# Kernel optimization log

Measured on AMD Instinct MI355X. Metric: run time of the kernel, lower is better.

The kernel has to match this reference:

```python
import jax, jax.numpy as jnp
import numpy as np

NUM_RELATIONS = 3


def _rgcn(x, W_rel, W_root, bias, src, dst, etype):
    # PyG RGCNConv: out = x @ W_root + bias + sum_r mean_{e: type(e)=r, dst(e)=i} (x_src @ W_r)
    n = x.shape[0]
    xr = jnp.einsum('ni,rio->rno', x, W_rel)          # [R, N, F] relation-transformed nodes
    msg = xr[etype, src]                               # [E, F] per-edge messages
    out = x @ W_root + bias
    for r in range(NUM_RELATIONS):
        m = (etype == r)
        s = jax.ops.segment_sum(jnp.where(m[:, None], msg, 0.0), dst, num_segments=n)
        c = jax.ops.segment_sum(m.astype(x.dtype), dst, num_segments=n)
        out = out + s / jnp.maximum(c, 1.0)[:, None]   # mean aggregation per relation
    return out


def _gate(h, q, Wg, bg, Wq, bq):
    # h: [BN, F], q: [B, L, F]
    B, L, F = q.shape
    N = h.shape[0] // B
    h3 = h.reshape(B, N, F)
    # w_gate(cat([h_i, q_l])) = h_i @ Wg[:, :F].T + q_l @ Wg[:, F:].T + bg
    hg = jnp.einsum('bnf,gf->bng', h3, Wg[:, :F])                    # [B,N,F]
    qg = jnp.einsum('blf,gf->blg', q, Wg[:, F:]) + bg                # [B,L,F]
    attn = jax.nn.sigmoid(hg[:, :, None, :] + qg[:, None, :, :])     # [B,N,L,F]
    qi = jnp.einsum('bnlf,blf->bnf', attn, q)                        # [B,N,F]
    alpha = jax.nn.sigmoid(
        jnp.einsum('bnf,gf->bng', h3, Wq[:, :F])
        + jnp.einsum('bnf,gf->bng', qi, Wq[:, F:]) + bq)
    hn = alpha * jnp.tanh(qi) + (1.0 - alpha) * h3
    return hn.reshape(B * N, F)


def setup_inputs() -> dict:
    key = jax.random.key(0)
    ks = jax.random.split(key, 16)
    F = 768
    BN, E, B, L = 2048, 65536, 8, 64
    s = 0.02
    return {
        'x': jax.random.normal(ks[0], (BN, F), jnp.float32),
        'edge_index': jax.random.randint(ks[1], (2, E), 0, BN),
        'edge_type': jax.random.randint(ks[2], (E,), 0, NUM_RELATIONS),
        'query_embs': jax.random.normal(ks[3], (B, L, F), jnp.float32),
        'W_rel1': jax.random.normal(ks[4], (NUM_RELATIONS, F, F), jnp.float32) * s,
        'W_root1': jax.random.normal(ks[5], (F, F), jnp.float32) * s,
        'b1': jnp.zeros((F,), jnp.float32),
        'W_rel2': jax.random.normal(ks[6], (NUM_RELATIONS, F, F), jnp.float32) * s,
        'W_root2': jax.random.normal(ks[7], (F, F), jnp.float32) * s,
        'b2': jnp.zeros((F,), jnp.float32),
        'Wg': jax.random.normal(ks[8], (F, 2 * F), jnp.float32) * s,
        'bg': jnp.zeros((F,), jnp.float32),
        'Wq': jax.random.normal(ks[9], (F, 2 * F), jnp.float32) * s,
        'bq': jnp.zeros((F,), jnp.float32),
    }


def reference(x, edge_index, edge_type, query_embs,
              W_rel1, W_root1, b1, W_rel2, W_root2, b2, Wg, bg, Wq, bq):
    src, dst = edge_index[0], edge_index[1]
    h = jax.nn.relu(_rgcn(x, W_rel1, W_root1, b1, src, dst, edge_type))
    h = _gate(h, query_embs, Wg, bg, Wq, bq)
    h = jax.nn.relu(_rgcn(h, W_rel2, W_root2, b2, src, dst, edge_type))
    h = _gate(h, query_embs, Wg, bg, Wq, bq)
    return h
```

## Files before the change

### kernel.cpp

```cpp
#include <hip/hip_runtime.h>
#include <hip/hip_bf16.h>
#include <cstdint>
#include <cstddef>

#define F 768

typedef float f32x4 __attribute__((ext_vector_type(4)));
typedef short s16x8 __attribute__((ext_vector_type(8)));
typedef short s16x4 __attribute__((ext_vector_type(4)));

#define NEG_LOG2E (-1.4426950408889634f)

__device__ __forceinline__ float bf2f(unsigned short u) {
  union { unsigned int i; float f; } v; v.i = ((unsigned int)u) << 16; return v.f;
}
__device__ __forceinline__ unsigned short f2bf(float f) {
  union { float f; unsigned int i; } v; v.f = f;
  unsigned int r = v.i + 0x7FFF + ((v.i >> 16) & 1);
  return (unsigned short)(r >> 16);
}

#if __has_builtin(__builtin_amdgcn_exp2f)
__device__ __forceinline__ float fexp2(float x) { return __builtin_amdgcn_exp2f(x); }
#else
__device__ __forceinline__ float fexp2(float x) { return exp2f(x); }
#endif
#if __has_builtin(__builtin_amdgcn_rcpf)
__device__ __forceinline__ float frcp(float x) { return __builtin_amdgcn_rcpf(x); }
#else
__device__ __forceinline__ float frcp(float x) { return 1.0f / x; }
#endif

__device__ __forceinline__ float ftanh(float x) {
  float t = fexp2(x * 2.8853900817779268f);
  float s = frcp(t + 1.0f);
  return fmaf(-2.0f, s, 1.0f);
}
__device__ __forceinline__ float fclamp60(float x) {
  return fminf(fmaxf(x, -60.0f), 60.0f);
}

__device__ __forceinline__ void gload16(const void* g, void* l) {
  __builtin_amdgcn_global_load_lds(
      (const __attribute__((address_space(1))) void*)g,
      (__attribute__((address_space(3))) void*)l, 16, 0, 0);
}

__global__ void khist(const int* __restrict__ ei, int E, int* __restrict__ cnt) {
  int e = blockIdx.x * blockDim.x + threadIdx.x;
  if (e < E) atomicAdd(&cnt[ei[E + e]], 1);
}

__global__ void kscan(const int* __restrict__ cnt, int* __restrict__ offs, int n) {
  __shared__ int part[256];
  int t = threadIdx.x;
  const int per = n / 256;
  int local[8];
  int s = 0;
  for (int j = 0; j < per; ++j) { local[j] = cnt[t * per + j]; s += local[j]; }
  part[t] = s;
  __syncthreads();
  for (int d = 1; d < 256; d <<= 1) {
    int v = (t >= d) ? part[t - d] : 0;
    __syncthreads();
    part[t] += v;
    __syncthreads();
  }
  int run = (t == 0) ? 0 : part[t - 1];
  for (int j = 0; j < per; ++j) { offs[t * per + j] = run; run += local[j]; }
  if (t == 255) offs[n] = run;
}

__global__ void kscatter(const int* __restrict__ ei, const int* __restrict__ et, int E,
                         const int* __restrict__ offs, int* __restrict__ cur,
                         int* __restrict__ sorted) {
  int e = blockIdx.x * blockDim.x + threadIdx.x;
  if (e >= E) return;
  int dst = ei[E + e];
  int pos = offs[dst] + atomicAdd(&cur[dst], 1);
  sorted[pos] = ei[e] | (et[e] << 16);
}

__global__ void kprep(const float* __restrict__ x, const float* __restrict__ q,
                      const float* __restrict__ Wg, const float* __restrict__ Wq,
                      int nx, int nq,
                      unsigned short* __restrict__ Acat, unsigned short* __restrict__ qbf,
                      unsigned short* __restrict__ Wgq, unsigned short* __restrict__ WgR,
                      unsigned short* __restrict__ WqR) {
  const int b = blockIdx.x, c = threadIdx.x * 4;
  const float* srow;
  unsigned short* drow;
  if (b < nx) {
    srow = x + (size_t)b * F; drow = Acat + (size_t)b * 3072;
  } else if (b < nx + nq) {
    srow = q + (size_t)(b - nx) * F; drow = qbf + (size_t)(b - nx) * F;
  } else {
    const int w = b - nx - nq;
    if (w < 1536) {
      srow = (w < 768) ? Wg + (size_t)w * 1536 : Wq + (size_t)(w - 768) * 1536;
      drow = Wgq + (size_t)w * 768;
    } else if (w < 2304) {
      srow = Wg + (size_t)(w - 1536) * 1536 + 768;
      drow = WgR + (size_t)(w - 1536) * 768;
    } else {
      srow = Wq + (size_t)(w - 2304) * 1536 + 768;
      drow = WqR + (size_t)(w - 2304) * 768;
    }
  }
  float4 v = *(const float4*)(srow + c);
  s16x4 o;
  o[0] = (short)f2bf(v.x); o[1] = (short)f2bf(v.y);
  o[2] = (short)f2bf(v.z); o[3] = (short)f2bf(v.w);
  *(s16x4*)(drow + c) = o;
}

__global__ void ktrans(const float* __restrict__ Wr1, const float* __restrict__ Wl1,
                       const float* __restrict__ Wr2, const float* __restrict__ Wl2,
                       unsigned short* __restrict__ Wcat1, unsigned short* __restrict__ Wcat2) {
  __shared__ float tile[64][65];
  const int z = blockIdx.z, layer = z >> 2, part = z & 3;
  const float* src = (part == 0) ? (layer ? Wr2 : Wr1)
                                 : ((layer ? Wl2 : Wl1) + (size_t)(part - 1) * F * F);
  unsigned short* dst = (layer ? Wcat2 : Wcat1) + part * F;
  const int kt = blockIdx.x * 64, nt = blockIdx.y * 64;
  const int t = threadIdx.x, c = t & 63, r4 = t >> 6;
#pragma unroll
  for (int it = 0; it < 16; ++it) {
    int kk = r4 + it * 4;
    tile[kk][c] = src[(size_t)(kt + kk) * F + nt + c];
  }
  __syncthreads();
#pragma unroll
  for (int it = 0; it < 16; ++it) {
    int rr = r4 + it * 4;
    dst[(size_t)(nt + rr) * 3072 + kt + c] = f2bf(tile[c][rr]);
  }
}

__global__ void kagg(const int* __restrict__ offs, const int* __restrict__ sorted,
                     const unsigned short* __restrict__ hin,
                     unsigned short* __restrict__ dst) {
  const int i = blockIdx.x, t = threadIdx.x;
  const int col = t * 4;
  float a0[4] = {}, a1[4] = {}, a2[4] = {};
  int c0 = 0, c1 = 0, c2 = 0;
  const int beg = offs[i], end = offs[i + 1];
  int e = beg;
  for (; e + 3 < end; e += 4) {
    int pk[4];
#pragma unroll
    for (int u = 0; u < 4; ++u) pk[u] = sorted[e + u];
    s16x4 w[4];
#pragma unroll
    for (int u = 0; u < 4; ++u)
      w[u] = *(const s16x4*)(hin + (size_t)(pk[u] & 0xFFFF) * 3072 + col);
#pragma unroll
    for (int u = 0; u < 4; ++u) {
      int r = pk[u] >> 16;
      float v[4];
#pragma unroll
      for (int j = 0; j < 4; ++j) v[j] = bf2f((unsigned short)w[u][j]);
      if (r == 0)      { c0++; for (int j = 0; j < 4; ++j) a0[j] += v[j]; }
      else if (r == 1) { c1++; for (int j = 0; j < 4; ++j) a1[j] += v[j]; }
      else             { c2++; for (int j = 0; j < 4; ++j) a2[j] += v[j]; }
    }
  }
  for (; e < end; ++e) {
    int p0 = sorted[e];
    s16x4 w0 = *(const s16x4*)(hin + (size_t)(p0 & 0xFFFF) * 3072 + col);
    int r0 = p0 >> 16;
    float v0[4];
#pragma unroll
    for (int j = 0; j < 4; ++j) v0[j] = bf2f((unsigned short)w0[j]);
    if (r0 == 0)      { c0++; for (int j = 0; j < 4; ++j) a0[j] += v0[j]; }
    else if (r0 == 1) { c1++; for (int j = 0; j < 4; ++j) a1[j] += v0[j]; }
    else              { c2++; for (int j = 0; j < 4; ++j) a2[j] += v0[j]; }
  }
  const float i0 = frcp((float)(c0 > 0 ? c0 : 1));
  const float i1 = frcp((float)(c1 > 0 ? c1 : 1));
  const float i2 = frcp((float)(c2 > 0 ? c2 : 1));
  unsigned short* d = dst + (size_t)i * 3072 + col;
  s16x4 o;
#pragma unroll
  for (int j = 0; j < 4; ++j) o[j] = (short)f2bf(a0[j] * i0);
  *(s16x4*)d = o;
#pragma unroll
  for (int j = 0; j < 4; ++j) o[j] = (short)f2bf(a1[j] * i1);
  *(s16x4*)(d + F) = o;
#pragma unroll
  for (int j = 0; j < 4; ++j) o[j] = (short)f2bf(a2[j] * i2);
  *(s16x4*)(d + 2 * F) = o;
}

template <int EPI>
__launch_bounds__(512)
__global__ void kmm(const unsigned short* __restrict__ A, int lda,
                    const unsigned short* __restrict__ B, int ldb,
                    float* __restrict__ C, int ldc, int K,
                    const float* __restrict__ bias,
                    const float* __restrict__ auxf,
                    const unsigned short* __restrict__ hbb,
                    unsigned short* __restrict__ C2, int ldc2,
                    unsigned short* __restrict__ tqb,
                    int Lq) {
  __shared__ unsigned short Asb[2][64 * 64];
  __shared__ unsigned short Bsb[2][64 * 64];
  const int t = threadIdx.x;
  const int lane = t & 63, wid = t >> 6;
  const int wr = wid >> 2, wc = wid & 3;
  const int bm = blockIdx.x * 64, bn = blockIdx.y * 64;

  const int srow = t >> 3, schunk = t & 7;
  const int kxor = ((schunk ^ (srow & 7)) << 3);
  const unsigned short* Ap = A + (size_t)(bm + srow) * lda + kxor;
  const unsigned short* Bp = B + (size_t)(bn + srow) * ldb + kxor;

  const int rA0 = wr * 32 + (lane & 15);
  const int rB0 = wc * 16 + (lane & 15);
  const int l7 = lane & 7, lq = lane >> 4;
  const int s8_0 = (((0 * 4 + lq) ^ l7) << 3);
  const int s8_1 = (((1 * 4 + lq) ^ l7) << 3);

  f32x4 acc[2] = {};

  auto stage = [&](int cb, int k0) {
    gload16(Ap + k0, &Asb[cb][t * 8]);
    gload16(Bp + k0, &Bsb[cb][t * 8]);
  };

  stage(0, 0);
  __syncthreads();
  int cur = 0;
  for (int k0 = 0; k0 < K; k0 += 64) {
    if (k0 + 64 < K) stage(cur ^ 1, k0 + 64);
    const unsigned short* As = Asb[cur];
    const unsigned short* Bs = Bsb[cur];
#pragma unroll
    for (int ks = 0; ks < 2; ++ks) {
      const int s8 = ks ? s8_1 : s8_0;
      s16x8 af[2], bf;
#pragma unroll
      for (int i = 0; i < 2; ++i)
        af[i] = *(const s16x8*)(As + (rA0 + i * 16) * 64 + s8);
      bf = *(const s16x8*)(Bs + rB0 * 64 + s8);
#pragma unroll
      for (int i = 0; i < 2; ++i)
        acc[i] = __builtin_amdgcn_mfma_f32_16x16x32_bf16(af[i], bf, acc[i], 0, 0, 0);
    }
    __syncthreads();
    cur ^= 1;
  }

  const int colw = bn + wc * 16 + (lane & 15);

  if (EPI == 7) {
    if (bn < 768) {
      float ea[2][4], qacc[2][4];
#pragma unroll
      for (int i = 0; i < 2; ++i)
#pragma unroll
        for (int j = 0; j < 4; ++j) {
          ea[i][j] = fexp2(fclamp60(acc[i][j] * NEG_LOG2E));
          qacc[i][j] = 0.0f;
        }
      const int b = bm >> 8;
      const float* qb = auxf + (size_t)b * Lq * F;
      const float* qeb = bias + (size_t)b * Lq * F;
#pragma unroll 4
      for (int l = 0; l < Lq; ++l) {
        const float qe = qeb[(size_t)l * F + colw];
        const float q0 = qb[(size_t)l * F + colw];
#pragma unroll
        for (int i = 0; i < 2; ++i)
#pragma unroll
          for (int j = 0; j < 4; ++j)
            qacc[i][j] = fmaf(frcp(fmaf(ea[i][j], qe, 1.0f)), q0, qacc[i][j]);
      }
#pragma unroll
      for (int i = 0; i < 2; ++i)
#pragma unroll
        for (int j = 0; j < 4; ++j) {
          const int row = bm + wr * 32 + i * 16 + (lane >> 4) * 4 + j;
          C2[(size_t)row * 768 + colw] = f2bf(qacc[i][j]);
          tqb[(size_t)row * 768 + colw] = f2bf(ftanh(qacc[i][j]));
        }
    } else {
#pragma unroll
      for (int i = 0; i < 2; ++i)
#pragma unroll
        for (int j = 0; j < 4; ++j) {
          const int row = bm + wr * 32 + i * 16 + (lane >> 4) * 4 + j;
          C[(size_t)row * 768 + (colw - 768)] = acc[i][j];
        }
    }
    return;
  }

#pragma unroll
  for (int i = 0; i < 2; ++i)
#pragma unroll
    for (int j = 0; j < 4; ++j) {
      const int row = bm + wr * 32 + i * 16 + (lane >> 4) * 4 + j;
      const int col = colw;
      float v = acc[i][j];
      if (EPI == 3 || EPI == 4) {
        float zh = auxf[(size_t)row * 768 + col];
        float z = v + bias[col] + zh;
        float al = frcp(1.0f + fexp2(z * NEG_LOG2E));
        float tq = bf2f(tqb[(size_t)row * 768 + col]);
        float hv = bf2f(hbb[(size_t)row * 768 + col]);
        float o = al * tq + (1.0f - al) * hv;
        if (EPI == 3) C2[(size_t)row * ldc2 + col] = f2bf(o);
        else          C[(size_t)row * ldc + col] = o;
      } else if (EPI == 6) {
        C[(size_t)row * ldc + col] = fexp2(fclamp60((v + bias[col]) * NEG_LOG2E));
      }
    }
}

__launch_bounds__(512)
__global__ void kmm_pk(const unsigned short* __restrict__ A, int lda,
                       const unsigned short* __restrict__ B, int ldb,
                       float* __restrict__ P, int Ksplit, int pstride) {
  __shared__ unsigned short Asb[2][64 * 64];
  __shared__ unsigned short Bsb[2][64 * 64];
  const int t = threadIdx.x;
  const int lane = t & 63, wid = t >> 6;
  const int wr = wid >> 2, wc = wid & 3;
  const int bm = blockIdx.x * 64, bn = blockIdx.y * 64;
  const int kbase = blockIdx.z * Ksplit;
  float* Cp = P + (size_t)blockIdx.z * pstride;

  const int srow = t >> 3, schunk = t & 7;
  const int kxor = ((schunk ^ (srow & 7)) << 3);
  const unsigned short* Ap = A + (size_t)(bm + srow) * lda + kxor + kbase;
  const unsigned short* Bp = B + (size_t)(bn + srow) * ldb + kxor + kbase;

  const int rA0 = wr * 32 + (lane & 15);
  const int rB0 = wc * 16 + (lane & 15);
  const int l7 = lane & 7, lq = lane >> 4;
  const int s8_0 = (((0 * 4 + lq) ^ l7) << 3);
  const int s8_1 = (((1 * 4 + lq) ^ l7) << 3);

  f32x4 acc[2] = {};

  auto stage = [&](int cb, int k0) {
    gload16(Ap + k0, &Asb[cb][t * 8]);
    gload16(Bp + k0, &Bsb[cb][t * 8]);
  };

  stage(0, 0);
  __syncthreads();
  int cur = 0;
  for (int k0 = 0; k0 < Ksplit; k0 += 64) {
    if (k0 + 64 < Ksplit) stage(cur ^ 1, k0 + 64);
    const unsigned short* As = Asb[cur];
    const unsigned short* Bs = Bsb[cur];
#pragma unroll
    for (int ks = 0; ks < 2; ++ks) {
      const int s8 = ks ? s8_1 : s8_0;
      s16x8 af[2], bf;
#pragma unroll
      for (int i = 0; i < 2; ++i)
        af[i] = *(const s16x8*)(As + (rA0 + i * 16) * 64 + s8);
      bf = *(const s16x8*)(Bs + rB0 * 64 + s8);
#pragma unroll
      for (int i = 0; i < 2; ++i)
        acc[i] = __builtin_amdgcn_mfma_f32_16x16x32_bf16(af[i], bf, acc[i], 0, 0, 0);
    }
    __syncthreads();
    cur ^= 1;
  }

  const int col = bn + wc * 16 + (lane & 15);
#pragma unroll
  for (int i = 0; i < 2; ++i)
#pragma unroll
    for (int j = 0; j < 4; ++j) {
      const int row = bm + wr * 32 + i * 16 + (lane >> 4) * 4 + j;
      Cp[(size_t)row * F + col] = acc[i][j];
    }
}

__global__ void kep_relu(const float* __restrict__ P, int pstride,
                         const float* __restrict__ bias,
                         unsigned short* __restrict__ hb) {
  const int idx = (blockIdx.x * 256 + threadIdx.x) * 4;
  const int col = idx - (idx / F) * F;
  float4 s = *(const float4*)(P + idx);
  const float4 s1 = *(const float4*)(P + pstride + idx);
  const float4 bv = *(const float4*)(bias + col);
  s.x = fmaxf(s.x + s1.x + bv.x, 0.0f);
  s.y = fmaxf(s.y + s1.y + bv.y, 0.0f);
  s.z = fmaxf(s.z + s1.z + bv.z, 0.0f);
  s.w = fmaxf(s.w + s1.w + bv.w, 0.0f);
  s16x4 o;
  o[0] = (short)f2bf(s.x); o[1] = (short)f2bf(s.y);
  o[2] = (short)f2bf(s.z); o[3] = (short)f2bf(s.w);
  *(s16x4*)(hb + idx) = o;
}

extern "C" void kernel_launch(void* const* d_in, const int* in_sizes, int n_in,
                              void* d_out, int out_size, void* d_ws, size_t ws_size,
                              hipStream_t stream) {
  const float* x = (const float*)d_in[0];
  const int* ei = (const int*)d_in[1];
  const int* et = (const int*)d_in[2];
  const float* q = (const float*)d_in[3];
  const float* Wrel1 = (const float*)d_in[4];
  const float* Wroot1 = (const float*)d_in[5];
  const float* b1 = (const float*)d_in[6];
  const float* Wrel2 = (const float*)d_in[7];
  const float* Wroot2 = (const float*)d_in[8];
  const float* b2 = (const float*)d_in[9];
  const float* Wg = (const float*)d_in[10];
  const float* bg = (const float*)d_in[11];
  const float* Wq = (const float*)d_in[12];
  const float* bq = (const float*)d_in[13];

  const int BNn = in_sizes[0] / F;
  const int E = in_sizes[1] / 2;
  const int L = 64;
  const int Bq = in_sizes[3] / (L * F);
  const int ML = Bq * L;
  const int PSTR = BNn * F;
  float* out = (float*)d_out;

  char* p = (char*)d_ws;
  auto alloc = [&](size_t bytes) {
    void* r = (void*)p;
    p += (bytes + 255) & ~(size_t)255;
    return r;
  };
  int* cntcur = (int*)alloc((size_t)2 * BNn * 4);
  int* cnt = cntcur;
  int* cur = cntcur + BNn;
  int* offs = (int*)alloc((size_t)(BNn + 1) * 4);
  int* sorted = (int*)alloc((size_t)E * 4);
  unsigned short* Acat = (unsigned short*)alloc((size_t)BNn * 3072 * 2);
  unsigned short* Wcat1 = (unsigned short*)alloc((size_t)F * 3072 * 2);
  unsigned short* Wcat2 = (unsigned short*)alloc((size_t)F * 3072 * 2);
  unsigned short* Wgq = (unsigned short*)alloc((size_t)1536 * F * 2);
  unsigned short* WgR = (unsigned short*)alloc((size_t)F * F * 2);
  unsigned short* WqR = (unsigned short*)alloc((size_t)F * F * 2);
  unsigned short* qbf = (unsigned short*)alloc((size_t)ML * F * 2);
  float* qgE = (float*)alloc((size_t)ML * F * 4);
  unsigned short* hb = (unsigned short*)alloc((size_t)BNn * F * 2);
  float* zhb = (float*)alloc((size_t)BNn * F * 4);
  unsigned short* tqb = (unsigned short*)alloc((size_t)BNn * F * 2);
  unsigned short* qib = (unsigned short*)alloc((size_t)BNn * F * 2);
  float* parts = (float*)alloc((size_t)2 * PSTR * 4);

  hipMemsetAsync(cntcur, 0, (size_t)2 * BNn * 4, stream);
  khist<<<(E + 255) / 256, 256, 0, stream>>>(ei, E, cnt);
  kscan<<<1, 256, 0, stream>>>(cnt, offs, BNn);
  kscatter<<<(E + 255) / 256, 256, 0, stream>>>(ei, et, E, offs, cur, sorted);

  kprep<<<BNn + ML + 3072, 192, 0, stream>>>(x, q, Wg, Wq, BNn, ML,
                                             Acat, qbf, Wgq, WgR, WqR);
  ktrans<<<dim3(12, 12, 8), 256, 0, stream>>>(Wroot1, Wrel1, Wroot2, Wrel2, Wcat1, Wcat2);

  kmm<6><<<dim3(ML / 64, F / 64), 512, 0, stream>>>(
      qbf, F, WgR, F, qgE, F, F, bg, nullptr, nullptr, nullptr, 0, nullptr, L);

  for (int layer = 0; layer < 2; ++layer) {
    const unsigned short* Wcat = layer ? Wcat2 : Wcat1;
    const float* bb = layer ? b2 : b1;

    kagg<<<BNn, 192, 0, stream>>>(offs, sorted, Acat, Acat + F);

    kmm_pk<<<dim3(BNn / 64, F / 64, 2), 512, 0, stream>>>(
        Acat, 3072, Wcat, 3072, parts, 1536, PSTR);

    kep_relu<<<(BNn * F) / 1024, 256, 0, stream>>>(parts, PSTR, bb, hb);

    kmm<7><<<dim3(BNn / 64, 1536 / 64), 512, 0, stream>>>(
        hb, F, Wgq, F, zhb, F, F, qgE, q, nullptr, qib, F, tqb, L);

    if (layer == 0) {
      kmm<3><<<dim3(BNn / 64, F / 64), 512, 0, stream>>>(
          qib, F, WqR, F, nullptr, 0, F, bq, zhb, hb, Acat, 3072, tqb, L);
    } else {
      kmm<4><<<dim3(BNn / 64, F / 64), 512, 0, stream>>>(
          qib, F, WqR, F, out, F, F, bq, zhb, hb, nullptr, 0, tqb, L);
    }
  }
}
```

Before: 291.2 us.

## Use 128x64 tiles for RGCN and gate GEMMs and fold histogram into prep

The split-K RGCN GEMM and the gate GEMM move from 64x64 to 128x64 block tiles, with each wave computing a 32x32 sub-tile (2x2 MFMAs). This doubles B-operand reuse per load and halves the block count. The gate epilogue now lives in a dedicated kmm7 kernel, and its loop over queries handles two column groups per load. The edge-degree histogram is merged into the kprep launch as extra blocks, removing one kernel launch. The cost is fewer blocks (less parallelism on a large GPU) and higher register pressure in the epilogue.

```diff
diff --git a/kernel.cpp b/kernel.cpp
--- a/kernel.cpp
+++ b/kernel.cpp
@@ -44,11 +44,6 @@
   __builtin_amdgcn_global_load_lds(
       (const __attribute__((address_space(1))) void*)g,
       (__attribute__((address_space(3))) void*)l, 16, 0, 0);
-}
-
-__global__ void khist(const int* __restrict__ ei, int E, int* __restrict__ cnt) {
-  int e = blockIdx.x * blockDim.x + threadIdx.x;
-  if (e < E) atomicAdd(&cnt[ei[E + e]], 1);
 }
 
 __global__ void kscan(const int* __restrict__ cnt, int* __restrict__ offs, int n) {
@@ -83,6 +78,7 @@
 
 __global__ void kprep(const float* __restrict__ x, const float* __restrict__ q,
                       const float* __restrict__ Wg, const float* __restrict__ Wq,
+                      const int* __restrict__ ei, int E, int* __restrict__ cnt,
                       int nx, int nq,
                       unsigned short* __restrict__ Acat, unsigned short* __restrict__ qbf,
                       unsigned short* __restrict__ Wgq, unsigned short* __restrict__ WgR,
@@ -94,7 +90,7 @@
     srow = x + (size_t)b * F; drow = Acat + (size_t)b * 3072;
   } else if (b < nx + nq) {
     srow = q + (size_t)(b - nx) * F; drow = qbf + (size_t)(b - nx) * F;
-  } else {
+  } else if (b < nx + nq + 3072) {
     const int w = b - nx - nq;
     if (w < 1536) {
       srow = (w < 768) ? Wg + (size_t)w * 1536 : Wq + (size_t)(w - 768) * 1536;
@@ -106,6 +102,11 @@
       srow = Wq + (size_t)(w - 2304) * 1536 + 768;
       drow = WqR + (size_t)(w - 2304) * 768;
     }
+  } else {
+    const int w2 = b - nx - nq - 3072;
+    for (int e = w2 * 192 + threadIdx.x; e < E; e += 256 * 192)
+      atomicAdd(&cnt[ei[E + e]], 1);
+    return;
   }
   float4 v = *(const float4*)(srow + c);
   s16x4 o;
@@ -201,8 +202,7 @@
                     const float* __restrict__ auxf,
                     const unsigned short* __restrict__ hbb,
                     unsigned short* __restrict__ C2, int ldc2,
-                    unsigned short* __restrict__ tqb,
-                    int Lq) {
+                    unsigned short* __restrict__ tqb) {
   __shared__ unsigned short Asb[2][64 * 64];
   __shared__ unsigned short Bsb[2][64 * 64];
   const int t = threadIdx.x;
@@ -252,50 +252,6 @@
   }
 
   const int colw = bn + wc * 16 + (lane & 15);
-
-  if (EPI == 7) {
-    if (bn < 768) {
-      float ea[2][4], qacc[2][4];
-#pragma unroll
-      for (int i = 0; i < 2; ++i)
-#pragma unroll
-        for (int j = 0; j < 4; ++j) {
-          ea[i][j] = fexp2(fclamp60(acc[i][j] * NEG_LOG2E));
-          qacc[i][j] = 0.0f;
-        }
-      const int b = bm >> 8;
-      const float* qb = auxf + (size_t)b * Lq * F;
-      const float* qeb = bias + (size_t)b * Lq * F;
-#pragma unroll 4
-      for (int l = 0; l < Lq; ++l) {
-        const float qe = qeb[(size_t)l * F + colw];
-        const float q0 = qb[(size_t)l * F + colw];
-#pragma unroll
-        for (int i = 0; i < 2; ++i)
-#pragma unroll
-          for (int j = 0; j < 4; ++j)
-            qacc[i][j] = fmaf(frcp(fmaf(ea[i][j], qe, 1.0f)), q0, qacc[i][j]);
-      }
-#pragma unroll
-      for (int i = 0; i < 2; ++i)
-#pragma unroll
-        for (int j = 0; j < 4; ++j) {
-          const int row = bm + wr * 32 + i * 16 + (lane >> 4) * 4 + j;
-          C2[(size_t)row * 768 + colw] = f2bf(qacc[i][j]);
-          tqb[(size_t)row * 768 + colw] = f2bf(ftanh(qacc[i][j]));
-        }
-    } else {
-#pragma unroll
-      for (int i = 0; i < 2; ++i)
-#pragma unroll
-        for (int j = 0; j < 4; ++j) {
-          const int row = bm + wr * 32 + i * 16 + (lane >> 4) * 4 + j;
-          C[(size_t)row * 768 + (colw - 768)] = acc[i][j];
-        }
-    }
-    return;
-  }
-
 #pragma unroll
   for (int i = 0; i < 2; ++i)
 #pragma unroll
@@ -318,68 +274,162 @@
     }
 }
 
+#define KMM128_BODY(AP_LO, AP_HI, BP, KLEN)                                        \
+  f32x4 acc[2][2] = {};                                                            \
+  auto stage = [&](int cb, int k0) {                                               \
+    gload16(AP_LO + k0, &Asb[cb][t * 8]);                                          \
+    gload16(AP_HI + k0, &Asb[cb][64 * 64 + t * 8]);                                \
+    gload16(BP + k0, &Bsb[cb][t * 8]);                                             \
+  };                                                                               \
+  stage(0, 0);                                                                     \
+  __syncthreads();                                                                 \
+  int cur = 0;                                                                     \
+  for (int k0 = 0; k0 < (KLEN); k0 += 64) {                                        \
+    if (k0 + 64 < (KLEN)) stage(cur ^ 1, k0 + 64);                                 \
+    const unsigned short* As = Asb[cur];                                           \
+    const unsigned short* Bs = Bsb[cur];                                           \
+    _Pragma("unroll")                                                              \
+    for (int ks = 0; ks < 2; ++ks) {                                               \
+      const int s8 = ks ? s8_1 : s8_0;                                             \
+      s16x8 af[2], bf[2];                                                          \
+      _Pragma("unroll")                                                            \
+      for (int i = 0; i < 2; ++i)                                                  \
+        af[i] = *(const s16x8*)(As + (rA0 + i * 16) * 64 + s8);                    \
+      _Pragma("unroll")                                                            \
+      for (int n = 0; n < 2; ++n)                                                  \
+        bf[n] = *(const s16x8*)(Bs + (rB0 + n * 16) * 64 + s8);                    \
+      _Pragma("unroll")                                                            \
+      for (int i = 0; i < 2; ++i)                                                  \
+        _Pragma("unroll")                                                          \
+        for (int n = 0; n < 2; ++n)                                                \
+          acc[i][n] = __builtin_amdgcn_mfma_f32_16x16x32_bf16(af[i], bf[n],        \
+                                                              acc[i][n], 0, 0, 0); \
+    }                                                                              \
+    __syncthreads();                                                               \
+    cur ^= 1;                                                                      \
+  }
+
 __launch_bounds__(512)
 __global__ void kmm_pk(const unsigned short* __restrict__ A, int lda,
                        const unsigned short* __restrict__ B, int ldb,
                        float* __restrict__ P, int Ksplit, int pstride) {
-  __shared__ unsigned short Asb[2][64 * 64];
+  __shared__ unsigned short Asb[2][128 * 64];
   __shared__ unsigned short Bsb[2][64 * 64];
   const int t = threadIdx.x;
   const int lane = t & 63, wid = t >> 6;
-  const int wr = wid >> 2, wc = wid & 3;
-  const int bm = blockIdx.x * 64, bn = blockIdx.y * 64;
+  const int wr = wid & 3, wc = wid >> 2;
+  const int bm = blockIdx.x * 128, bn = blockIdx.y * 64;
   const int kbase = blockIdx.z * Ksplit;
   float* Cp = P + (size_t)blockIdx.z * pstride;
 
   const int srow = t >> 3, schunk = t & 7;
   const int kxor = ((schunk ^ (srow & 7)) << 3);
-  const unsigned short* Ap = A + (size_t)(bm + srow) * lda + kxor + kbase;
+  const unsigned short* ApLo = A + (size_t)(bm + srow) * lda + kxor + kbase;
+  const unsigned short* ApHi = A + (size_t)(bm + 64 + srow) * lda + kxor + kbase;
   const unsigned short* Bp = B + (size_t)(bn + srow) * ldb + kxor + kbase;
 
   const int rA0 = wr * 32 + (lane & 15);
-  const int rB0 = wc * 16 + (lane & 15);
+  const int rB0 = wc * 32 + (lane & 15);
   const int l7 = lane & 7, lq = lane >> 4;
   const int s8_0 = (((0 * 4 + lq) ^ l7) << 3);
   const int s8_1 = (((1 * 4 + lq) ^ l7) << 3);
 
-  f32x4 acc[2] = {};
-
-  auto stage = [&](int cb, int k0) {
-    gload16(Ap + k0, &Asb[cb][t * 8]);
-    gload16(Bp + k0, &Bsb[cb][t * 8]);
-  };
-
-  stage(0, 0);
-  __syncthreads();
-  int cur = 0;
-  for (int k0 = 0; k0 < Ksplit; k0 += 64) {
-    if (k0 + 64 < Ksplit) stage(cur ^ 1, k0 + 64);
-    const unsigned short* As = Asb[cur];
-    const unsigned short* Bs = Bsb[cur];
-#pragma unroll
-    for (int ks = 0; ks < 2; ++ks) {
-      const int s8 = ks ? s8_1 : s8_0;
-      s16x8 af[2], bf;
+  KMM128_BODY(ApLo, ApHi, Bp, Ksplit)
+
+#pragma unroll
+  for (int i = 0; i < 2; ++i)
+#pragma unroll
+    for (int n = 0; n < 2; ++n)
+#pragma unroll
+      for (int j = 0; j < 4; ++j) {
+        const int row = bm + wr * 32 + i * 16 + (lane >> 4) * 4 + j;
+        const int col = bn + wc * 32 + n * 16 + (lane & 15);
+        Cp[(size_t)row * F + col] = acc[i][n][j];
+      }
+}
+
+__launch_bounds__(512)
+__global__ void kmm7(const unsigned short* __restrict__ A, int lda,
+                     const unsigned short* __restrict__ B, int ldb,
+                     float* __restrict__ zhb,
+                     const float* __restrict__ qgE,
+                     const float* __restrict__ qraw,
+                     unsigned short* __restrict__ qib,
+                     unsigned short* __restrict__ tqb, int Lq) {
+  __shared__ unsigned short Asb[2][128 * 64];
+  __shared__ unsigned short Bsb[2][64 * 64];
+  const int t = threadIdx.x;
+  const int lane = t & 63, wid = t >> 6;
+  const int wr = wid & 3, wc = wid >> 2;
+  const int bm = blockIdx.x * 128, bn = blockIdx.y * 64;
+
+  const int srow = t >> 3, schunk = t & 7;
+  const int kxor = ((schunk ^ (srow & 7)) << 3);
+  const unsigned short* ApLo = A + (size_t)(bm + srow) * lda + kxor;
+  const unsigned short* ApHi = A + (size_t)(bm + 64 + srow) * lda + kxor;
+  const unsigned short* Bp = B + (size_t)(bn + srow) * ldb + kxor;
+
+  const int rA0 = wr * 32 + (lane & 15);
+  const int rB0 = wc * 32 + (lane & 15);
+  const int l7 = lane & 7, lq = lane >> 4;
+  const int s8_0 = (((0 * 4 + lq) ^ l7) << 3);
+  const int s8_1 = (((1 * 4 + lq) ^ l7) << 3);
+
+  KMM128_BODY(ApLo, ApHi, Bp, 768)
+
+  const int colw = bn + wc * 32 + (lane & 15);
+
+  if (bn < 768) {
+    float ea[2][2][4], qacc[2][2][4];
+#pragma unroll
+    for (int i = 0; i < 2; ++i)
+#pragma unroll
+      for (int n = 0; n < 2; ++n)
+#pragma unroll
+        for (int j = 0; j < 4; ++j) {
+          ea[i][n][j] = fexp2(fclamp60(acc[i][n][j] * NEG_LOG2E));
+          qacc[i][n][j] = 0.0f;
+        }
+    const int b = bm >> 8;
+    const float* qb = qraw + (size_t)b * Lq * F;
+    const float* qeb = qgE + (size_t)b * Lq * F;
+#pragma unroll 2
+    for (int l = 0; l < Lq; ++l) {
+      const float qe0 = qeb[(size_t)l * F + colw];
+      const float qe1 = qeb[(size_t)l * F + colw + 16];
+      const float q0 = qb[(size_t)l * F + colw];
+      const float q1 = qb[(size_t)l * F + colw + 16];
 #pragma unroll
       for (int i = 0; i < 2; ++i)
-        af[i] = *(const s16x8*)(As + (rA0 + i * 16) * 64 + s8);
-      bf = *(const s16x8*)(Bs + rB0 * 64 + s8);
-#pragma unroll
-      for (int i = 0; i < 2; ++i)
-        acc[i] = __builtin_amdgcn_mfma_f32_16x16x32_bf16(af[i], bf, acc[i], 0, 0, 0);
+#pragma unroll
+        for (int j = 0; j < 4; ++j) {
+          qacc[i][0][j] = fmaf(frcp(fmaf(ea[i][0][j], qe0, 1.0f)), q0, qacc[i][0][j]);
+          qacc[i][1][j] = fmaf(frcp(fmaf(ea[i][1][j], qe1, 1.0f)), q1, qacc[i][1][j]);
+        }
     }
-    __syncthreads();
-    cur ^= 1;
-  }
-
-  const int col = bn + wc * 16 + (lane & 15);
-#pragma unroll
-  for (int i = 0; i < 2; ++i)
-#pragma unroll
-    for (int j = 0; j < 4; ++j) {
-      const int row = bm + wr * 32 + i * 16 + (lane >> 4) * 4 + j;
-      Cp[(size_t)row * F + col] = acc[i][j];
-    }
+#pragma unroll
+    for (int i = 0; i < 2; ++i)
+#pragma unroll
+      for (int n = 0; n < 2; ++n)
+#pragma unroll
+        for (int j = 0; j < 4; ++j) {
+          const int row = bm + wr * 32 + i * 16 + (lane >> 4) * 4 + j;
+          const int col = colw + n * 16;
+          qib[(size_t)row * 768 + col] = f2bf(qacc[i][n][j]);
+          tqb[(size_t)row * 768 + col] = f2bf(ftanh(qacc[i][n][j]));
+        }
+  } else {
+#pragma unroll
+    for (int i = 0; i < 2; ++i)
+#pragma unroll
+      for (int n = 0; n < 2; ++n)
+#pragma unroll
+        for (int j = 0; j < 4; ++j) {
+          const int row = bm + wr * 32 + i * 16 + (lane >> 4) * 4 + j;
+          const int col = colw + n * 16 - 768;
+          zhb[(size_t)row * 768 + col] = acc[i][n][j];
+        }
+  }
 }
 
 __global__ void kep_relu(const float* __restrict__ P, int pstride,
@@ -452,16 +502,14 @@
   float* parts = (float*)alloc((size_t)2 * PSTR * 4);
 
   hipMemsetAsync(cntcur, 0, (size_t)2 * BNn * 4, stream);
-  khist<<<(E + 255) / 256, 256, 0, stream>>>(ei, E, cnt);
+  kprep<<<BNn + ML + 3072 + 256, 192, 0, stream>>>(x, q, Wg, Wq, ei, E, cnt, BNn, ML,
+                                                   Acat, qbf, Wgq, WgR, WqR);
   kscan<<<1, 256, 0, stream>>>(cnt, offs, BNn);
   kscatter<<<(E + 255) / 256, 256, 0, stream>>>(ei, et, E, offs, cur, sorted);
-
-  kprep<<<BNn + ML + 3072, 192, 0, stream>>>(x, q, Wg, Wq, BNn, ML,
-                                             Acat, qbf, Wgq, WgR, WqR);
   ktrans<<<dim3(12, 12, 8), 256, 0, stream>>>(Wroot1, Wrel1, Wroot2, Wrel2, Wcat1, Wcat2);
 
   kmm<6><<<dim3(ML / 64, F / 64), 512, 0, stream>>>(
-      qbf, F, WgR, F, qgE, F, F, bg, nullptr, nullptr, nullptr, 0, nullptr, L);
+      qbf, F, WgR, F, qgE, F, F, bg, nullptr, nullptr, nullptr, 0, nullptr);
 
   for (int layer = 0; layer < 2; ++layer) {
     const unsigned short* Wcat = layer ? Wcat2 : Wcat1;
@@ -469,20 +517,20 @@
 
     kagg<<<BNn, 192, 0, stream>>>(offs, sorted, Acat, Acat + F);
 
-    kmm_pk<<<dim3(BNn / 64, F / 64, 2), 512, 0, stream>>>(
+    kmm_pk<<<dim3(BNn / 128, F / 64, 2), 512, 0, stream>>>(
         Acat, 3072, Wcat, 3072, parts, 1536, PSTR);
 
     kep_relu<<<(BNn * F) / 1024, 256, 0, stream>>>(parts, PSTR, bb, hb);
 
-    kmm<7><<<dim3(BNn / 64, 1536 / 64), 512, 0, stream>>>(
-        hb, F, Wgq, F, zhb, F, F, qgE, q, nullptr, qib, F, tqb, L);
+    kmm7<<<dim3(BNn / 128, 1536 / 64), 512, 0, stream>>>(
+        hb, F, Wgq, F, zhb, qgE, q, qib, tqb, L);
 
     if (layer == 0) {
       kmm<3><<<dim3(BNn / 64, F / 64), 512, 0, stream>>>(
-          qib, F, WqR, F, nullptr, 0, F, bq, zhb, hb, Acat, 3072, tqb, L);
+          qib, F, WqR, F, nullptr, 0, F, bq, zhb, hb, Acat, 3072, tqb);
     } else {
       kmm<4><<<dim3(BNn / 64, F / 64), 512, 0, stream>>>(
-          qib, F, WqR, F, out, F, F, bq, zhb, hb, nullptr, 0, tqb, L);
+          qib, F, WqR, F, out, F, F, bq, zhb, hb, nullptr, 0, tqb);
     }
   }
 }
```

Result: slower. 310.7 us (+6.7%).
